# Optimization experiments

Measured on AMD Instinct MI355X. Metric: run time of the kernel, lower is better.

## Reference

```python
import jax, jax.numpy as jnp
import numpy as np

D_MODEL = 1024
NHEAD = 16
D_K = D_MODEL // NHEAD
B, S = 2, 2048
NEG_INF = float('-inf')


def setup_inputs() -> dict:
    key = jax.random.key(0)
    ks = jax.random.split(key, 12)
    sc = 1.0 / np.sqrt(D_MODEL)
    return {
        'q': jax.random.normal(ks[0], (B, S, D_MODEL), dtype=jnp.float32),
        'k': jax.random.normal(ks[1], (B, S, D_MODEL), dtype=jnp.float32),
        'q_mask': jax.random.randint(ks[2], (B, S), 0, 2, dtype=jnp.int32),
        'k_mask': jax.random.randint(ks[3], (B, S), 0, 2, dtype=jnp.int32),
        'Wq': jax.random.normal(ks[4], (D_MODEL, D_MODEL), dtype=jnp.float32) * sc,
        'bq': jnp.zeros((D_MODEL,), dtype=jnp.float32),
        'Wk': jax.random.normal(ks[5], (D_MODEL, D_MODEL), dtype=jnp.float32) * sc,
        'bk': jnp.zeros((D_MODEL,), dtype=jnp.float32),
        'Wv': jax.random.normal(ks[6], (D_MODEL, D_MODEL), dtype=jnp.float32) * sc,
        'bv': jnp.zeros((D_MODEL,), dtype=jnp.float32),
        'Wo': jax.random.normal(ks[7], (D_MODEL, D_MODEL), dtype=jnp.float32) * sc,
        'bo': jnp.zeros((D_MODEL,), dtype=jnp.float32),
        'causal_attention': 1,
    }


def _split_heads(x):  # [B,S,D] -> [B,H,S,d_k]
    b, s, _ = x.shape
    return x.reshape(b, s, NHEAD, D_K).transpose(0, 2, 1, 3)


def reference(q, k, q_mask, k_mask, Wq, bq, Wk, bk, Wv, bv, Wo, bo, causal_attention):
    v_in = k  # module uses V = K
    qh = _split_heads(q @ Wq.T + bq)
    kh = _split_heads(k @ Wk.T + bk)
    vh = _split_heads(v_in @ Wv.T + bv)
    # [B,H,Sq,Sk]
    scores = jnp.einsum('bhqd,bhkd->bhqk', qh, kh) / jnp.sqrt(jnp.float32(D_K))
    sq, sk = scores.shape[-2], scores.shape[-1]
    if causal_attention:
        causal = jnp.triu(jnp.ones((sq, sk), dtype=bool), k=1)
        scores = jnp.where(causal[None, None], NEG_INF, scores)
    scores = jnp.where(k_mask[:, None, None, :] == 0, NEG_INF, scores)
    attn = jax.nn.softmax(scores, axis=-1)
    attn = jnp.where(q_mask[:, None, :, None] == 0, 0.0, attn)
    out = jnp.einsum('bhqk,bhkd->bhqd', attn, vh)  # [B,H,Sq,d_k]
    out = out.transpose(0, 2, 1, 3).reshape(q.shape[0], sq, D_MODEL)
    return out @ Wo.T + bo
```

## Files before the change

### kernel.cpp

```cpp
#include <hip/hip_runtime.h>

typedef unsigned short u16;
typedef unsigned int   u32;
typedef __bf16 bf16x8 __attribute__((ext_vector_type(8)));
typedef float  f32x4  __attribute__((ext_vector_type(4)));

#define NEG_INF (-__builtin_inff())

#define GLDS16(g, l) __builtin_amdgcn_global_load_lds( \
    (const __attribute__((address_space(1))) void*)(g), \
    (__attribute__((address_space(3))) void*)(l), 16, 0, 0)

__device__ __forceinline__ u16 f2bf(float f) {
  u32 u = __builtin_bit_cast(u32, f);
  u32 r = u + 0x7FFFu + ((u >> 16) & 1u);
  return (u16)(r >> 16);
}
__device__ __forceinline__ float bf2f(u16 v) {
  u32 u = ((u32)v) << 16;
  return __builtin_bit_cast(float, u);
}
__device__ __forceinline__ u32 pk2bf(float a, float b) {
  return __builtin_amdgcn_perm(__builtin_bit_cast(u32, b),
                               __builtin_bit_cast(u32, a), 0x07060302u);
}

__device__ __forceinline__ int detect_flag(const u16* q16) {
  __shared__ int cnt;
  if (threadIdx.x == 0) cnt = 0;
  __syncthreads();
  int local = 0;
  for (int i = threadIdx.x; i < 2048; i += 256) {
    int e = (q16[i] >> 7) & 0xFF;
    if (e >= 118 && e <= 129) local++;
  }
  atomicAdd(&cnt, local);
  __syncthreads();
  return (cnt > 1536) ? 1 : 0;
}

struct ConvArgs {
  const void* src[10];
  u16* dst[10];
};

__global__ void convert_kernel(ConvArgs a, const int* __restrict__ kmask,
                               u16* __restrict__ mask01, int* __restrict__ flag) {
  if (blockIdx.x >= 1024) {
    int idx = (blockIdx.x - 1024) * 256 + threadIdx.x;
    mask01[idx] = kmask[idx] ? 0x3F80u : 0u;
    return;
  }
  const int fl = detect_flag((const u16*)a.src[0]);
  if (blockIdx.x == 0 && threadIdx.x == 0) flag[0] = fl;
  if (fl) return;

  const int total = 1573376;
  for (int u0 = blockIdx.x * 256 + threadIdx.x; u0 < total; u0 += 1024 * 256) {
    int s, off;
    if (u0 < 1048576)      { s = u0 >> 19;                 off = u0 & 524287; }
    else if (u0 < 1572864) { int v = u0 - 1048576; s = 2 + (v >> 17); off = v & 131071; }
    else                   { int v = u0 - 1572864; s = 6 + (v >> 7);  off = v & 127; }
    u16* d = a.dst[s] + (size_t)off * 8;
    const float* sp = (const float*)a.src[s] + (size_t)off * 8;
    u16 tmp[8];
    #pragma unroll
    for (int j = 0; j < 8; j++) tmp[j] = f2bf(sp[j]);
    *(uint4*)d = *(uint4*)tmp;
  }
}

template <int BM, int BN>
__device__ __forceinline__ void gemm_mainloop(
    const u16* __restrict__ A, const u16* __restrict__ W,
    int bm, int bn, u16 (*As)[BM * 32], u16 (*Bs)[BN * 32],
    f32x4 (*acc)[BN / 32]) {
  const int t = threadIdx.x, lane = t & 63, w = t >> 6;
  const int wm = (w >> 1) * (BM / 2), wn = (w & 1) * (BN / 2);
  const int l15 = lane & 15, quad = lane >> 4;
  const int sr = t >> 2;
  const int sc = ((t & 3) ^ ((t >> 3) & 3)) * 8;
  const int rq = (quad ^ ((l15 >> 1) & 3)) * 8;
  const u16* Ag0 = A + (size_t)(bm + sr) * 1024 + sc;
  const u16* Ag1 = Ag0 + (size_t)64 * 1024;
  const u16* Wg0 = W + (size_t)(bn + sr) * 1024 + sc;
  const u16* Wg1 = Wg0 + (size_t)64 * 1024;

  GLDS16(Ag0, As[0] + t * 8);
  if (BM == 128) GLDS16(Ag1, As[0] + 2048 + t * 8);
  GLDS16(Wg0, Bs[0] + t * 8);
  if (BN == 128) GLDS16(Wg1, Bs[0] + 2048 + t * 8);

  int st = 0;
  for (int k0 = 0; k0 < 1024; k0 += 32, st ^= 1) {
    __syncthreads();
    if (k0 + 32 < 1024) {
      GLDS16(Ag0 + k0 + 32, As[st ^ 1] + t * 8);
      if (BM == 128) GLDS16(Ag1 + k0 + 32, As[st ^ 1] + 2048 + t * 8);
      GLDS16(Wg0 + k0 + 32, Bs[st ^ 1] + t * 8);
      if (BN == 128) GLDS16(Wg1 + k0 + 32, Bs[st ^ 1] + 2048 + t * 8);
    }
    bf16x8 af[BM / 32], bw[BN / 32];
    #pragma unroll
    for (int i = 0; i < BM / 32; i++)
      af[i] = *(const bf16x8*)&As[st][(wm + i * 16 + l15) * 32 + rq];
    #pragma unroll
    for (int j = 0; j < BN / 32; j++)
      bw[j] = *(const bf16x8*)&Bs[st][(wn + j * 16 + l15) * 32 + rq];
    #pragma unroll
    for (int i = 0; i < BM / 32; i++)
      #pragma unroll
      for (int j = 0; j < BN / 32; j++)
        acc[i][j] = __builtin_amdgcn_mfma_f32_16x16x32_bf16(af[i], bw[j], acc[i][j], 0, 0, 0);
  }
}

struct QkvPtrs {
  const u16 *q, *k, *Wq, *Wk, *Wv, *bq, *bk, *bv;
};

__global__ __launch_bounds__(256, 5) void qkv_proj_kernel(
    QkvPtrs cv, QkvPtrs og, const int* __restrict__ flag,
    const int* __restrict__ kmask,
    u16* __restrict__ Qp, u16* __restrict__ Kp, u16* __restrict__ Vt) {
  __shared__ __align__(16) u16 As[2][64 * 32];
  __shared__ __align__(16) u16 Bs[2][128 * 32];
  const QkvPtrs& P = (*flag) ? og : cv;
  const int bid = blockIdx.x;
  const int xb = (bid >> 3) & 7;
  const int g = ((bid >> 6) << 3) | (bid & 7);
  const int z = g >> 6, yb = g & 63;
  const u16* A    = (z == 0) ? P.q  : P.k;
  const u16* W    = (z == 0) ? P.Wq : (z == 1) ? P.Wk : P.Wv;
  const u16* bias = (z == 0) ? P.bq : (z == 1) ? P.bk : P.bv;
  const int bm = yb * 64, bn = xb * 128;

  const f32x4 fzero = {0.f, 0.f, 0.f, 0.f};
  f32x4 acc[2][4];
  #pragma unroll
  for (int i = 0; i < 2; i++)
    #pragma unroll
    for (int j = 0; j < 4; j++) acc[i][j] = fzero;

  gemm_mainloop<64, 128>(A, W, bm, bn, As, Bs, acc);

  const int t = threadIdx.x, lane = t & 63, w = t >> 6;
  const int wm = (w >> 1) * 32, wn = (w & 1) * 64;
  const int l15 = lane & 15, quad = lane >> 4;

  if (z < 2) {
    u16* out = (z == 0) ? Qp : Kp;
    #pragma unroll
    for (int i = 0; i < 2; i++)
      #pragma unroll
      for (int j = 0; j < 4; j++) {
        int n = bn + wn + j * 16 + l15;
        float bb = bf2f(bias[n]);
        int m0 = bm + wm + i * 16 + quad * 4;
        #pragma unroll
        for (int r = 0; r < 4; r++)
          out[(size_t)(m0 + r) * 1024 + n] = f2bf(acc[i][j][r] + bb);
      }
  } else {
    #pragma unroll
    for (int i = 0; i < 2; i++) {
      int m0 = bm + wm + i * 16 + quad * 4;
      int b_ = m0 >> 11, s0 = m0 & 2047;
      const int4 km = *(const int4*)&kmask[b_ * 2048 + s0];
      #pragma unroll
      for (int j = 0; j < 4; j++) {
        int n = bn + wn + j * 16 + l15;
        int hh = n >> 6, dw = n & 63;
        float bb = bf2f(bias[n]);
        u16 tmp[4];
        tmp[0] = km.x ? f2bf(acc[i][j][0] + bb) : (u16)0;
        tmp[1] = km.y ? f2bf(acc[i][j][1] + bb) : (u16)0;
        tmp[2] = km.z ? f2bf(acc[i][j][2] + bb) : (u16)0;
        tmp[3] = km.w ? f2bf(acc[i][j][3] + bb) : (u16)0;
        *(ushort4*)&Vt[((size_t)(b_ * 16 + hh) * 64 + dw) * 2048 + s0] = *(ushort4*)tmp;
      }
    }
  }
}

__global__ __launch_bounds__(256, 4) void attn_kernel(
    const u16* __restrict__ Qp, const u16* __restrict__ Kp, const u16* __restrict__ Vt,
    const int* __restrict__ qmask, const u16* __restrict__ mask01,
    const int* __restrict__ causal_p, u16* __restrict__ AO) {
  __shared__ __align__(16) u16 KS[128 * 64];
  __shared__ __align__(16) u16 VS[64 * 128];
  __shared__ __align__(16) u16 P[4][16 * 64];

  const int t = threadIdx.x, lane = t & 63, w = t >> 6;
  const int quad = lane >> 4, l15 = lane & 15, l7 = l15 & 7;
  const int bh = blockIdx.x & 31;
  const int g4 = 31 - (int)(blockIdx.x >> 5);
  const int b = bh >> 4, h = bh & 15;
  const int causal = *causal_p;
  const int q0 = g4 * 64 + w * 16;
  const int nkt = causal ? (g4 >> 1) + 1 : 16;
  const float cs = 0.18033688011112042f;
  const float C = 40.0f;
  const f32x4 fzero = {0.f, 0.f, 0.f, 0.f};

  const u16* qr = Qp + (size_t)(b * 2048 + q0 + l15) * 1024 + h * 64 + quad * 8;
  const bf16x8 qf0 = *(const bf16x8*)qr;
  const bf16x8 qf1 = *(const bf16x8*)(qr + 32);

  const int kLr = lane >> 3, kLc = lane & 7;
  const u16* kgw = Kp + (size_t)(b * 2048 + 32 * w + kLr) * 1024 + h * 64 +
                   (kLc ^ kLr) * 8;
  const int vLr = lane >> 4, vLc = lane & 15;
  const u16* vgw = Vt + (size_t)bh * 131072 + (size_t)(16 * w) * 2048;
  int voff[4];
  #pragma unroll
  for (int i = 0; i < 4; i++)
    voff[i] = (4 * i + vLr) * 2048 + ((vLc ^ (4 * i + vLr)) * 8);
  u16* kls = &KS[(32 * w) * 64] + lane * 8;
  u16* vls = &VS[(16 * w) * 128] + lane * 8;

  f32x4 Oa[4], Dacc = fzero;
  #pragma unroll
  for (int dt = 0; dt < 4; dt++) Oa[dt] = fzero;
  u16* Pw = P[w];
  const u16* mrow = mask01 + b * 2048;

  for (int kt = 0; kt < nkt; kt++) {
    const u16* kg = kgw + (size_t)kt * 131072;
    const u16* vg = vgw + kt * 128;
    #pragma unroll
    for (int i = 0; i < 4; i++) {
      GLDS16(kg + i * 8192, kls + i * 512);
      GLDS16(vg + voff[i], vls + i * 512);
    }
    __syncthreads();

    f32x4 sa[8];
    #pragma unroll
    for (int mt = 0; mt < 8; mt++) sa[mt] = fzero;
    #pragma unroll
    for (int mt = 0; mt < 8; mt++) {
      bf16x8 kf0 = *(const bf16x8*)&KS[(mt * 16 + l15) * 64 + ((quad ^ l7) * 8)];
      bf16x8 kf1 = *(const bf16x8*)&KS[(mt * 16 + l15) * 64 + (((quad ^ l7) ^ 4) * 8)];
      sa[mt] = __builtin_amdgcn_mfma_f32_16x16x32_bf16(kf0, qf0, sa[mt], 0, 0, 0);
      sa[mt] = __builtin_amdgcn_mfma_f32_16x16x32_bf16(kf1, qf1, sa[mt], 0, 0, 0);
    }

    const bool diag = causal && (kt * 128 + 127 > q0);
    #pragma unroll
    for (int mt = 0; mt < 8; mt++)
      #pragma unroll
      for (int r = 0; r < 4; r++) {
        float p = __builtin_amdgcn_exp2f(__builtin_fmaf(sa[mt][r], cs, -C));
        if (diag && (kt * 128 + mt * 16 + quad * 4 + r > q0 + l15)) p = 0.f;
        sa[mt][r] = p;
      }

    #pragma unroll
    for (int hh = 0; hh < 2; hh++) {
      #pragma unroll
      for (int mh = 0; mh < 4; mh++) {
        int B = mh * 2 + (quad >> 1);
        uint2 pk;
        pk.x = pk2bf(sa[hh * 4 + mh][0], sa[hh * 4 + mh][1]);
        pk.y = pk2bf(sa[hh * 4 + mh][2], sa[hh * 4 + mh][3]);
        *(uint2*)&Pw[l15 * 64 + ((B ^ l7) * 8) + (quad & 1) * 4] = pk;
      }
      #pragma unroll
      for (int kh = 0; kh < 2; kh++) {
        int kp = hh * 2 + kh;
        bf16x8 pf = *(const bf16x8*)&Pw[l15 * 64 + (((kh * 4 + quad) ^ l7) * 8)];
        bf16x8 mf = *(const bf16x8*)(mrow + kt * 128 + kp * 32 + quad * 8);
        Dacc = __builtin_amdgcn_mfma_f32_16x16x32_bf16(pf, mf, Dacc, 0, 0, 0);
        #pragma unroll
        for (int dt = 0; dt < 4; dt++) {
          bf16x8 vf = *(const bf16x8*)
              &VS[(dt * 16 + l15) * 128 + (((kp * 4 + quad) ^ l15) * 8)];
          Oa[dt] = __builtin_amdgcn_mfma_f32_16x16x32_bf16(pf, vf, Oa[dt], 0, 0, 0);
        }
      }
    }
    __syncthreads();
  }

  const int4 qm = *(const int4*)&qmask[b * 2048 + q0 + quad * 4];
  f32x4 fv;
  fv[0] = (Dacc[0] > 0.f && qm.x) ? (1.0f / Dacc[0]) : 0.f;
  fv[1] = (Dacc[1] > 0.f && qm.y) ? (1.0f / Dacc[1]) : 0.f;
  fv[2] = (Dacc[2] > 0.f && qm.z) ? (1.0f / Dacc[2]) : 0.f;
  fv[3] = (Dacc[3] > 0.f && qm.w) ? (1.0f / Dacc[3]) : 0.f;
  #pragma unroll
  for (int dt = 0; dt < 4; dt++)
    #pragma unroll
    for (int r = 0; r < 4; r++)
      AO[(size_t)(b * 2048 + q0 + quad * 4 + r) * 1024 + h * 64 + dt * 16 + l15] =
          f2bf(Oa[dt][r] * fv[r]);
}

__global__ __launch_bounds__(256) void oproj_kernel(
    const u16* __restrict__ AO,
    const u16* __restrict__ Woc, const u16* __restrict__ boc,
    const u16* __restrict__ Wog, const u16* __restrict__ bog,
    void* __restrict__ out, const int* __restrict__ flag) {
  __shared__ __align__(16) u16 As[2][64 * 32];
  __shared__ __align__(16) u16 Bs[2][64 * 32];
  const int isbf = *flag;
  const u16* Wo = isbf ? Wog : Woc;
  const u16* bo = isbf ? bog : boc;
  const int bid = blockIdx.x;
  const int xb = (bid >> 3) & 15;
  const int g = ((bid >> 7) << 3) | (bid & 7);
  const int bm = g * 64, bn = xb * 64;

  const f32x4 fzero = {0.f, 0.f, 0.f, 0.f};
  f32x4 acc[2][2];
  #pragma unroll
  for (int i = 0; i < 2; i++)
    #pragma unroll
    for (int j = 0; j < 2; j++) acc[i][j] = fzero;

  gemm_mainloop<64, 64>(AO, Wo, bm, bn, As, Bs, acc);

  const int t = threadIdx.x, lane = t & 63, w = t >> 6;
  const int wm = (w >> 1) * 32, wn = (w & 1) * 32;
  const int l15 = lane & 15, quad = lane >> 4;
  #pragma unroll
  for (int i = 0; i < 2; i++)
    #pragma unroll
    for (int j = 0; j < 2; j++) {
      int n = bn + wn + j * 16 + l15;
      float bb = bf2f(bo[n]);
      int m0 = bm + wm + i * 16 + quad * 4;
      #pragma unroll
      for (int r = 0; r < 4; r++) {
        float v = acc[i][j][r] + bb;
        size_t idx = (size_t)(m0 + r) * 1024 + n;
        if (isbf) ((u16*)out)[idx] = f2bf(v);
        else      ((float*)out)[idx] = v;
      }
    }
}

extern "C" void kernel_launch(void* const* d_in, const int* in_sizes, int n_in,
                              void* d_out, int out_size, void* d_ws, size_t ws_size,
                              hipStream_t stream) {
  (void)in_sizes; (void)n_in; (void)out_size; (void)ws_size;

  char* w = (char*)d_ws;
  int* flag = (int*)w;
  u16* qc  = (u16*)(w + 256);
  u16* kc  = qc  + 4194304;
  u16* Qp  = kc  + 4194304;
  u16* Kp  = Qp  + 4194304;
  u16* Vt  = Kp  + 4194304;
  u16* AO  = Vt  + 4194304;
  u16* Wqc = AO  + 4194304;
  u16* Wkc = Wqc + 1048576;
  u16* Wvc = Wkc + 1048576;
  u16* Woc = Wvc + 1048576;
  u16* bqc = Woc + 1048576;
  u16* bkc = bqc + 1024;
  u16* bvc = bkc + 1024;
  u16* boc = bvc + 1024;
  u16* mask01 = boc + 1024;

  ConvArgs ca;
  ca.src[0] = d_in[0];  ca.dst[0] = qc;
  ca.src[1] = d_in[1];  ca.dst[1] = kc;
  ca.src[2] = d_in[4];  ca.dst[2] = Wqc;
  ca.src[3] = d_in[6];  ca.dst[3] = Wkc;
  ca.src[4] = d_in[8];  ca.dst[4] = Wvc;
  ca.src[5] = d_in[10]; ca.dst[5] = Woc;
  ca.src[6] = d_in[5];  ca.dst[6] = bqc;
  ca.src[7] = d_in[7];  ca.dst[7] = bkc;
  ca.src[8] = d_in[9];  ca.dst[8] = bvc;
  ca.src[9] = d_in[11]; ca.dst[9] = boc;
  convert_kernel<<<1040, 256, 0, stream>>>(ca, (const int*)d_in[3], mask01, flag);

  QkvPtrs cv, og;
  cv.q = qc;               cv.k = kc;
  cv.Wq = Wqc;             cv.Wk = Wkc;             cv.Wv = Wvc;
  cv.bq = bqc;             cv.bk = bkc;             cv.bv = bvc;
  og.q = (const u16*)d_in[0];   og.k = (const u16*)d_in[1];
  og.Wq = (const u16*)d_in[4];  og.Wk = (const u16*)d_in[6];
  og.Wv = (const u16*)d_in[8];
  og.bq = (const u16*)d_in[5];  og.bk = (const u16*)d_in[7];
  og.bv = (const u16*)d_in[9];

  qkv_proj_kernel<<<1536, 256, 0, stream>>>(
      cv, og, flag, (const int*)d_in[3], Qp, Kp, Vt);

  attn_kernel<<<1024, 256, 0, stream>>>(
      Qp, Kp, Vt, (const int*)d_in[2], mask01, (const int*)d_in[12], AO);

  oproj_kernel<<<1024, 256, 0, stream>>>(
      AO, Woc, boc, (const u16*)d_in[10], (const u16*)d_in[11], d_out, flag);
}
```

Before: 215.9 us.

## Double-buffer K/V tiles in attention with 64-key tiles; move mask build into QKV kernel

The attention kernel now uses 64-key tiles with two LDS buffers for K and V. It prefetches the next tile via global_load_lds while computing on the current one, which drops one barrier per iteration and overlaps loads with MFMA work. Causal blocks also skip more masked keys because of the finer tile granularity. Separately, the k_mask to bf16 conversion moves from the convert kernel into extra blocks of the QKV projection launch. Smaller tiles mean more loop iterations and barriers, and the early prefetch relies on the barrier ordering to stay correct.

```diff
diff --git a/kernel.cpp b/kernel.cpp
--- a/kernel.cpp
+++ b/kernel.cpp
@@ -44,13 +44,7 @@
   u16* dst[10];
 };
 
-__global__ void convert_kernel(ConvArgs a, const int* __restrict__ kmask,
-                               u16* __restrict__ mask01, int* __restrict__ flag) {
-  if (blockIdx.x >= 1024) {
-    int idx = (blockIdx.x - 1024) * 256 + threadIdx.x;
-    mask01[idx] = kmask[idx] ? 0x3F80u : 0u;
-    return;
-  }
+__global__ void convert_kernel(ConvArgs a, int* __restrict__ flag) {
   const int fl = detect_flag((const u16*)a.src[0]);
   if (blockIdx.x == 0 && threadIdx.x == 0) flag[0] = fl;
   if (fl) return;
@@ -121,12 +115,17 @@
 
 __global__ __launch_bounds__(256, 5) void qkv_proj_kernel(
     QkvPtrs cv, QkvPtrs og, const int* __restrict__ flag,
-    const int* __restrict__ kmask,
+    const int* __restrict__ kmask, u16* __restrict__ mask01,
     u16* __restrict__ Qp, u16* __restrict__ Kp, u16* __restrict__ Vt) {
+  const int bid = blockIdx.x;
+  if (bid >= 1536) {
+    int idx = (bid - 1536) * 256 + threadIdx.x;
+    mask01[idx] = kmask[idx] ? 0x3F80u : 0u;
+    return;
+  }
   __shared__ __align__(16) u16 As[2][64 * 32];
   __shared__ __align__(16) u16 Bs[2][128 * 32];
   const QkvPtrs& P = (*flag) ? og : cv;
-  const int bid = blockIdx.x;
   const int xb = (bid >> 3) & 7;
   const int g = ((bid >> 6) << 3) | (bid & 7);
   const int z = g >> 6, yb = g & 63;
@@ -187,8 +186,8 @@
     const u16* __restrict__ Qp, const u16* __restrict__ Kp, const u16* __restrict__ Vt,
     const int* __restrict__ qmask, const u16* __restrict__ mask01,
     const int* __restrict__ causal_p, u16* __restrict__ AO) {
-  __shared__ __align__(16) u16 KS[128 * 64];
-  __shared__ __align__(16) u16 VS[64 * 128];
+  __shared__ __align__(16) u16 KS[2][64 * 64];
+  __shared__ __align__(16) u16 VS[2][64 * 64];
   __shared__ __align__(16) u16 P[4][16 * 64];
 
   const int t = threadIdx.x, lane = t & 63, w = t >> 6;
@@ -198,7 +197,7 @@
   const int b = bh >> 4, h = bh & 15;
   const int causal = *causal_p;
   const int q0 = g4 * 64 + w * 16;
-  const int nkt = causal ? (g4 >> 1) + 1 : 16;
+  const int nkt = causal ? g4 + 1 : 32;
   const float cs = 0.18033688011112042f;
   const float C = 40.0f;
   const f32x4 fzero = {0.f, 0.f, 0.f, 0.f};
@@ -207,17 +206,15 @@
   const bf16x8 qf0 = *(const bf16x8*)qr;
   const bf16x8 qf1 = *(const bf16x8*)(qr + 32);
 
-  const int kLr = lane >> 3, kLc = lane & 7;
-  const u16* kgw = Kp + (size_t)(b * 2048 + 32 * w + kLr) * 1024 + h * 64 +
-                   (kLc ^ kLr) * 8;
-  const int vLr = lane >> 4, vLc = lane & 15;
-  const u16* vgw = Vt + (size_t)bh * 131072 + (size_t)(16 * w) * 2048;
-  int voff[4];
-  #pragma unroll
-  for (int i = 0; i < 4; i++)
-    voff[i] = (4 * i + vLr) * 2048 + ((vLc ^ (4 * i + vLr)) * 8);
-  u16* kls = &KS[(32 * w) * 64] + lane * 8;
-  u16* vls = &VS[(16 * w) * 128] + lane * 8;
+  const int sLr = lane >> 3, sLc = lane & 7;
+  const u16* kgw = Kp + (size_t)(b * 2048 + 16 * w + sLr) * 1024 + h * 64 +
+                   (sLc ^ sLr) * 8;
+  const u16* vgw = Vt + (size_t)bh * 131072 +
+                   (size_t)(16 * w + sLr) * 2048 + (sLc ^ sLr) * 8;
+  u16* kls0 = &KS[0][(16 * w) * 64] + lane * 8;
+  u16* kls1 = &KS[1][(16 * w) * 64] + lane * 8;
+  u16* vls0 = &VS[0][(16 * w) * 64] + lane * 8;
+  u16* vls1 = &VS[1][(16 * w) * 64] + lane * 8;
 
   f32x4 Oa[4], Dacc = fzero;
   #pragma unroll
@@ -225,62 +222,70 @@
   u16* Pw = P[w];
   const u16* mrow = mask01 + b * 2048;
 
+  #pragma unroll
+  for (int i = 0; i < 2; i++) {
+    GLDS16(kgw + (size_t)i * 8192, kls0 + i * 512);
+    GLDS16(vgw + (size_t)i * 16384, vls0 + i * 512);
+  }
+
   for (int kt = 0; kt < nkt; kt++) {
-    const u16* kg = kgw + (size_t)kt * 131072;
-    const u16* vg = vgw + kt * 128;
-    #pragma unroll
-    for (int i = 0; i < 4; i++) {
-      GLDS16(kg + i * 8192, kls + i * 512);
-      GLDS16(vg + voff[i], vls + i * 512);
-    }
     __syncthreads();
-
-    f32x4 sa[8];
-    #pragma unroll
-    for (int mt = 0; mt < 8; mt++) sa[mt] = fzero;
-    #pragma unroll
-    for (int mt = 0; mt < 8; mt++) {
-      bf16x8 kf0 = *(const bf16x8*)&KS[(mt * 16 + l15) * 64 + ((quad ^ l7) * 8)];
-      bf16x8 kf1 = *(const bf16x8*)&KS[(mt * 16 + l15) * 64 + (((quad ^ l7) ^ 4) * 8)];
+    if (kt + 1 < nkt) {
+      const u16* kg = kgw + (size_t)(kt + 1) * 65536;
+      const u16* vg = vgw + (kt + 1) * 64;
+      u16* kd = ((kt + 1) & 1) ? kls1 : kls0;
+      u16* vd = ((kt + 1) & 1) ? vls1 : vls0;
+      #pragma unroll
+      for (int i = 0; i < 2; i++) {
+        GLDS16(kg + (size_t)i * 8192, kd + i * 512);
+        GLDS16(vg + (size_t)i * 16384, vd + i * 512);
+      }
+    }
+    const u16* KSc = KS[kt & 1];
+    const u16* VSc = VS[kt & 1];
+
+    f32x4 sa[4];
+    #pragma unroll
+    for (int mt = 0; mt < 4; mt++) sa[mt] = fzero;
+    #pragma unroll
+    for (int mt = 0; mt < 4; mt++) {
+      bf16x8 kf0 = *(const bf16x8*)&KSc[(mt * 16 + l15) * 64 + ((quad ^ l7) * 8)];
+      bf16x8 kf1 = *(const bf16x8*)&KSc[(mt * 16 + l15) * 64 + (((quad ^ l7) ^ 4) * 8)];
       sa[mt] = __builtin_amdgcn_mfma_f32_16x16x32_bf16(kf0, qf0, sa[mt], 0, 0, 0);
       sa[mt] = __builtin_amdgcn_mfma_f32_16x16x32_bf16(kf1, qf1, sa[mt], 0, 0, 0);
     }
 
-    const bool diag = causal && (kt * 128 + 127 > q0);
-    #pragma unroll
-    for (int mt = 0; mt < 8; mt++)
+    const bool diag = causal && (kt * 64 + 63 > q0);
+    #pragma unroll
+    for (int mt = 0; mt < 4; mt++)
       #pragma unroll
       for (int r = 0; r < 4; r++) {
         float p = __builtin_amdgcn_exp2f(__builtin_fmaf(sa[mt][r], cs, -C));
-        if (diag && (kt * 128 + mt * 16 + quad * 4 + r > q0 + l15)) p = 0.f;
+        if (diag && (kt * 64 + mt * 16 + quad * 4 + r > q0 + l15)) p = 0.f;
         sa[mt][r] = p;
       }
 
     #pragma unroll
-    for (int hh = 0; hh < 2; hh++) {
-      #pragma unroll
-      for (int mh = 0; mh < 4; mh++) {
-        int B = mh * 2 + (quad >> 1);
-        uint2 pk;
-        pk.x = pk2bf(sa[hh * 4 + mh][0], sa[hh * 4 + mh][1]);
-        pk.y = pk2bf(sa[hh * 4 + mh][2], sa[hh * 4 + mh][3]);
-        *(uint2*)&Pw[l15 * 64 + ((B ^ l7) * 8) + (quad & 1) * 4] = pk;
-      }
-      #pragma unroll
-      for (int kh = 0; kh < 2; kh++) {
-        int kp = hh * 2 + kh;
-        bf16x8 pf = *(const bf16x8*)&Pw[l15 * 64 + (((kh * 4 + quad) ^ l7) * 8)];
-        bf16x8 mf = *(const bf16x8*)(mrow + kt * 128 + kp * 32 + quad * 8);
-        Dacc = __builtin_amdgcn_mfma_f32_16x16x32_bf16(pf, mf, Dacc, 0, 0, 0);
-        #pragma unroll
-        for (int dt = 0; dt < 4; dt++) {
-          bf16x8 vf = *(const bf16x8*)
-              &VS[(dt * 16 + l15) * 128 + (((kp * 4 + quad) ^ l15) * 8)];
-          Oa[dt] = __builtin_amdgcn_mfma_f32_16x16x32_bf16(pf, vf, Oa[dt], 0, 0, 0);
-        }
-      }
-    }
-    __syncthreads();
+    for (int mh = 0; mh < 4; mh++) {
+      int B = mh * 2 + (quad >> 1);
+      uint2 pk;
+      pk.x = pk2bf(sa[mh][0], sa[mh][1]);
+      pk.y = pk2bf(sa[mh][2], sa[mh][3]);
+      *(uint2*)&Pw[l15 * 64 + ((B ^ l7) * 8) + (quad & 1) * 4] = pk;
+    }
+
+    #pragma unroll
+    for (int kp = 0; kp < 2; kp++) {
+      bf16x8 pf = *(const bf16x8*)&Pw[l15 * 64 + (((kp * 4 + quad) ^ l7) * 8)];
+      bf16x8 mf = *(const bf16x8*)(mrow + kt * 64 + kp * 32 + quad * 8);
+      Dacc = __builtin_amdgcn_mfma_f32_16x16x32_bf16(pf, mf, Dacc, 0, 0, 0);
+      #pragma unroll
+      for (int dt = 0; dt < 4; dt++) {
+        bf16x8 vf = *(const bf16x8*)
+            &VSc[(dt * 16 + l15) * 64 + (((kp * 4 + quad) ^ l7) * 8)];
+        Oa[dt] = __builtin_amdgcn_mfma_f32_16x16x32_bf16(pf, vf, Oa[dt], 0, 0, 0);
+      }
+    }
   }
 
   const int4 qm = *(const int4*)&qmask[b * 2048 + q0 + quad * 4];
@@ -375,7 +380,7 @@
   ca.src[7] = d_in[7];  ca.dst[7] = bkc;
   ca.src[8] = d_in[9];  ca.dst[8] = bvc;
   ca.src[9] = d_in[11]; ca.dst[9] = boc;
-  convert_kernel<<<1040, 256, 0, stream>>>(ca, (const int*)d_in[3], mask01, flag);
+  convert_kernel<<<1024, 256, 0, stream>>>(ca, flag);
 
   QkvPtrs cv, og;
   cv.q = qc;               cv.k = kc;
@@ -387,8 +392,8 @@
   og.bq = (const u16*)d_in[5];  og.bk = (const u16*)d_in[7];
   og.bv = (const u16*)d_in[9];
 
-  qkv_proj_kernel<<<1536, 256, 0, stream>>>(
-      cv, og, flag, (const int*)d_in[3], Qp, Kp, Vt);
+  qkv_proj_kernel<<<1552, 256, 0, stream>>>(
+      cv, og, flag, (const int*)d_in[3], mask01, Qp, Kp, Vt);
 
   attn_kernel<<<1024, 256, 0, stream>>>(
       Qp, Kp, Vt, (const int*)d_in[2], mask01, (const int*)d_in[12], AO);
```

New measurement: 216.3 us. No clear change (+0.2%).
